# Performance work log

Hardware: AMD Instinct MI355X
Metric: run time of the kernel (lower is better)

## Reference

```python
import jax, jax.numpy as jnp
import numpy as np

NEG_SLOPE = 0.2  # PyG GATConv default leaky_relu slope


def _gat_conv(x, src, dst, W, a_src, a_dst, b, num_nodes, heads, out_dim):
    # x: [N, F_in] -> h: [N, H, C]
    h = (x @ W).reshape(num_nodes, heads, out_dim)
    alpha_src = jnp.sum(h * a_src, axis=-1)  # [N, H]
    alpha_dst = jnp.sum(h * a_dst, axis=-1)  # [N, H]
    # per-edge unnormalized attention logits [E, H]
    alpha = jax.nn.leaky_relu(alpha_src[src] + alpha_dst[dst], NEG_SLOPE)
    # segment softmax over incoming edges of each destination node
    amax = jax.ops.segment_max(alpha, dst, num_segments=num_nodes)  # [N, H]
    e = jnp.exp(alpha - amax[dst])
    denom = jax.ops.segment_sum(e, dst, num_segments=num_nodes)  # [N, H]
    attn = e / denom[dst]  # every node has a self-loop, denom > 0
    # scatter-aggregate messages [E, H, C] -> [N, H, C]
    msg = h[src] * attn[:, :, None]
    out = jax.ops.segment_sum(msg, dst, num_segments=num_nodes)
    return out.reshape(num_nodes, heads * out_dim) + b


def setup_inputs() -> dict:
    key = jax.random.key(0)
    ks = jax.random.split(key, 12)
    N, F_in, H, C1, C2 = 100000, 128, 4, 32, 16
    E = 1600000
    x = jax.random.normal(ks[0], (N, F_in), dtype=jnp.float32)
    edge_index = jax.random.randint(ks[1], (2, E), 0, N, dtype=jnp.int64)
    s1 = 1.0 / np.sqrt(F_in)
    s2 = 1.0 / np.sqrt(H * C1)
    W1 = jax.random.normal(ks[2], (F_in, H * C1), dtype=jnp.float32) * s1
    a_src1 = jax.random.normal(ks[3], (H, C1), dtype=jnp.float32) * s1
    a_dst1 = jax.random.normal(ks[4], (H, C1), dtype=jnp.float32) * s1
    b1 = jnp.zeros((H * C1,), dtype=jnp.float32)
    W2 = jax.random.normal(ks[5], (H * C1, C2), dtype=jnp.float32) * s2
    a_src2 = jax.random.normal(ks[6], (1, C2), dtype=jnp.float32) * s2
    a_dst2 = jax.random.normal(ks[7], (1, C2), dtype=jnp.float32) * s2
    b2 = jnp.zeros((C2,), dtype=jnp.float32)
    return {"x": x, "edge_index": edge_index, "W1": W1, "a_src1": a_src1,
            "a_dst1": a_dst1, "b1": b1, "W2": W2, "a_src2": a_src2,
            "a_dst2": a_dst2, "b2": b2}


def reference(x, edge_index, W1, a_src1, a_dst1, b1, W2, a_src2, a_dst2, b2):
    N = x.shape[0]
    H, C1 = a_src1.shape
    C2 = a_src2.shape[1]
    # PyG GATConv default add_self_loops=True
    loop = jnp.arange(N, dtype=edge_index.dtype)
    src = jnp.concatenate([edge_index[0], loop])
    dst = jnp.concatenate([edge_index[1], loop])
    # dropout_ratio=0.0 / eval mode -> F.dropout is identity
    h = _gat_conv(x, src, dst, W1, a_src1, a_dst1, b1, N, H, C1)
    h = jax.nn.elu(h)
    out = _gat_conv(h, src, dst, W2, a_src2, a_dst2, b2, N, 1, C2)
    return out
```

## Files before the change

### kernel.cpp

```cpp
#include <hip/hip_runtime.h>
#include <cstdint>
#include <cstddef>

#define NEG_SLOPE 0.2f


__device__ __forceinline__ int edge_at(const void* ei, long long idx, int is64) {
    if (is64) return (int)((const long long*)ei)[idx];
    return ((const int*)ei)[idx];
}

__global__ void detect_fmt_kernel(const void* ei, int* flag) {
    if (threadIdx.x == 0 && blockIdx.x == 0) {
        const unsigned* u = (const unsigned*)ei;
        int zc = 0;
        for (int i = 0; i < 128; ++i) zc += (u[2 * i + 1] == 0u);
        *flag = (zc >= 100) ? 1 : 0;
    }
}

__global__ __launch_bounds__(256) void gemm1_kernel(
    const float* __restrict__ x, const float* __restrict__ W,
    const float* __restrict__ a_src, const float* __restrict__ a_dst,
    float* __restrict__ h1, float* __restrict__ asrc, float* __restrict__ adst,
    int N) {
    __shared__ float As2[32][132];
    __shared__ float Bs[32][128];
    const int tid = threadIdx.x;
    const int tx = tid & 15, ty = tid >> 4;
    const int base = blockIdx.x * 128;

    float acc[8][8];
#pragma unroll
    for (int i = 0; i < 8; ++i)
#pragma unroll
        for (int j = 0; j < 8; ++j) acc[i][j] = 0.f;

    for (int kb = 0; kb < 128; kb += 32) {
        {
            const int r0 = tid >> 3;
            const int q  = tid & 7;
#pragma unroll
            for (int p = 0; p < 4; ++p) {
                int r = r0 + p * 32;
                int gr = base + r;
                float4 v = make_float4(0.f, 0.f, 0.f, 0.f);
                if (gr < N) v = *(const float4*)(x + (size_t)gr * 128 + kb + q * 4);
                As2[q * 4 + 0][r] = v.x; As2[q * 4 + 1][r] = v.y;
                As2[q * 4 + 2][r] = v.z; As2[q * 4 + 3][r] = v.w;
            }
        }
        {
            const int k0 = tid >> 5;
            const int f  = tid & 31;
#pragma unroll
            for (int p = 0; p < 4; ++p) {
                int kk = k0 + p * 8;
                float4 v = *(const float4*)(W + (size_t)(kb + kk) * 128 + f * 4);
                *(float4*)&Bs[kk][f * 4] = v;
            }
        }
        __syncthreads();
#pragma unroll 4
        for (int kk = 0; kk < 32; ++kk) {
            float4 a0 = *(const float4*)&As2[kk][ty * 8];
            float4 a1 = *(const float4*)&As2[kk][ty * 8 + 4];
            float a[8] = {a0.x, a0.y, a0.z, a0.w, a1.x, a1.y, a1.z, a1.w};
            float4 b0 = *(const float4*)&Bs[kk][tx * 4];
            float4 b1 = *(const float4*)&Bs[kk][64 + tx * 4];
            float b[8] = {b0.x, b0.y, b0.z, b0.w, b1.x, b1.y, b1.z, b1.w};
#pragma unroll
            for (int i = 0; i < 8; ++i)
#pragma unroll
                for (int j = 0; j < 8; ++j)
                    acc[i][j] = fmaf(a[i], b[j], acc[i][j]);
        }
        __syncthreads();
    }

    float asv[8], adv[8];
#pragma unroll
    for (int jj = 0; jj < 4; ++jj) {
        asv[jj]     = a_src[tx * 4 + jj];
        asv[4 + jj] = a_src[64 + tx * 4 + jj];
        adv[jj]     = a_dst[tx * 4 + jj];
        adv[4 + jj] = a_dst[64 + tx * 4 + jj];
    }

#pragma unroll
    for (int i = 0; i < 8; ++i) {
        int gr = base + ty * 8 + i;
        float p0s = 0.f, p1s = 0.f, p0d = 0.f, p1d = 0.f;
#pragma unroll
        for (int jj = 0; jj < 4; ++jj) {
            p0s = fmaf(acc[i][jj],     asv[jj],     p0s);
            p0d = fmaf(acc[i][jj],     adv[jj],     p0d);
            p1s = fmaf(acc[i][4 + jj], asv[4 + jj], p1s);
            p1d = fmaf(acc[i][4 + jj], adv[4 + jj], p1d);
        }
#pragma unroll
        for (int off = 1; off < 8; off <<= 1) {
            p0s += __shfl_xor(p0s, off);
            p0d += __shfl_xor(p0d, off);
            p1s += __shfl_xor(p1s, off);
            p1d += __shfl_xor(p1d, off);
        }
        if (gr < N) {
            float4 o0 = make_float4(acc[i][0], acc[i][1], acc[i][2], acc[i][3]);
            float4 o1 = make_float4(acc[i][4], acc[i][5], acc[i][6], acc[i][7]);
            *(float4*)(h1 + (size_t)gr * 128 + tx * 4) = o0;
            *(float4*)(h1 + (size_t)gr * 128 + 64 + tx * 4) = o1;
            if ((tx & 7) == 0) {
                int hlo = tx >> 3;
                asrc[gr * 4 + hlo]     = p0s;
                adst[gr * 4 + hlo]     = p0d;
                asrc[gr * 4 + 2 + hlo] = p1s;
                adst[gr * 4 + 2 + hlo] = p1d;
            }
        }
    }
}

__global__ void deg_init_kernel(int* deg, int* cursor, int N) {
    int i = blockIdx.x * 256 + threadIdx.x;
    if (i < N) { deg[i] = 1; cursor[i] = 0; }
}

__global__ void hist_kernel(const void* ei, int* deg, int E, const int* flag) {
    int i = blockIdx.x * 256 + threadIdx.x;
    if (i < E) {
        int is64 = *flag;
        int d = edge_at(ei, (long long)E + i, is64);
        atomicAdd(&deg[d], 1);
    }
}

__global__ void reduce_kernel(const int* __restrict__ deg, int* bsums, int N) {
    __shared__ int s[256];
    int tid = threadIdx.x;
    int base = blockIdx.x * 1024 + tid * 4;
    int t = 0;
#pragma unroll
    for (int u = 0; u < 4; ++u) { int idx = base + u; if (idx < N) t += deg[idx]; }
    s[tid] = t;
    __syncthreads();
    for (int off = 128; off; off >>= 1) {
        if (tid < off) s[tid] += s[tid + off];
        __syncthreads();
    }
    if (tid == 0) bsums[blockIdx.x] = s[0];
}

__global__ void scan_bsums_kernel(int* bsums, int* rowptr, int nb, int N) {
    __shared__ int s[128];
    __shared__ int carry;
    int tid = threadIdx.x;
    if (tid == 0) carry = 0;
    __syncthreads();
    for (int base = 0; base < nb; base += 128) {
        int idx = base + tid;
        int v = (idx < nb) ? bsums[idx] : 0;
        s[tid] = v;
        __syncthreads();
        for (int off = 1; off < 128; off <<= 1) {
            int t = (tid >= off) ? s[tid - off] : 0;
            __syncthreads();
            s[tid] += t;
            __syncthreads();
        }
        int excl = carry + ((tid == 0) ? 0 : s[tid - 1]);
        if (idx < nb) bsums[idx] = excl;
        __syncthreads();
        if (tid == 0) carry += s[127];
        __syncthreads();
    }
    if (tid == 0) rowptr[N] = carry;
}

__global__ void scan_write_kernel(const int* __restrict__ deg,
                                  const int* __restrict__ bsums,
                                  int* __restrict__ rowptr, int N) {
    __shared__ int s[256];
    int tid = threadIdx.x;
    int base_i = blockIdx.x * 1024 + tid * 4;
    int v[4]; int t = 0;
#pragma unroll
    for (int u = 0; u < 4; ++u) {
        int idx = base_i + u;
        v[u] = (idx < N) ? deg[idx] : 0;
        t += v[u];
    }
    s[tid] = t;
    __syncthreads();
    for (int off = 1; off < 256; off <<= 1) {
        int tv = (tid >= off) ? s[tid - off] : 0;
        __syncthreads();
        s[tid] += tv;
        __syncthreads();
    }
    int excl = (tid == 0) ? 0 : s[tid - 1];
    int p = bsums[blockIdx.x] + excl;
#pragma unroll
    for (int u = 0; u < 4; ++u) {
        int idx = base_i + u;
        if (idx < N) rowptr[idx] = p;
        p += v[u];
    }
}

__global__ void scatter_kernel(const void* ei, const int* __restrict__ rowptr,
                               int* cursor, int* __restrict__ srcs,
                               int E, int ET, const int* flag) {
    int i = blockIdx.x * 256 + threadIdx.x;
    if (i < ET) {
        int is64 = *flag;
        int s, d;
        if (i < E) {
            s = edge_at(ei, i, is64);
            d = edge_at(ei, (long long)E + i, is64);
        } else {
            s = d = i - E;
        }
        int pos = rowptr[d] + atomicAdd(&cursor[d], 1);
        srcs[pos] = s;
    }
}

__global__ __launch_bounds__(128) void agg1_kernel(
    const float* __restrict__ h1, const float* __restrict__ asrc,
    const float* __restrict__ adst, const int* __restrict__ rowptr,
    const int* __restrict__ srcs, const float* __restrict__ b1,
    float* __restrict__ g, int N) {
    __shared__ float2 ws[4][36];
    int d = blockIdx.x;
    int tid = threadIdx.x;
    int h = tid >> 5, l = tid & 31;
    int start = rowptr[d], end = rowptr[d + 1];
    int deg = end - start;
    float ad = adst[d * 4 + h];

    float m = -1e30f;
    for (int j = start + l; j < end; j += 32) {
        float t = asrc[srcs[j] * 4 + h] + ad;
        t = (t > 0.f) ? t : NEG_SLOPE * t;
        m = fmaxf(m, t);
    }
#pragma unroll
    for (int off = 16; off; off >>= 1) m = fmaxf(m, __shfl_xor(m, off, 32));

    float a0 = 0.f, a1 = 0.f, a2 = 0.f, a3 = 0.f;
    float a4 = 0.f, a5 = 0.f, a6 = 0.f, a7 = 0.f;
    float lsum = 0.f;
    const float* h1c = h1 + tid;
    for (int cb = 0; cb < deg; cb += 32) {
        int cl = min(32, deg - cb);
        float wv = 0.f; int sv = 0;
        if (l < cl) {
            sv = srcs[start + cb + l];
            float t = asrc[sv * 4 + h] + ad;
            t = (t > 0.f) ? t : NEG_SLOPE * t;
            wv = __expf(t - m);
        }
        ws[h][l] = make_float2(wv, __int_as_float(sv));
        lsum += wv;
        int e = 0;
        for (; e + 8 <= cl; e += 8) {
            float2 p0 = ws[h][e + 0], p1 = ws[h][e + 1];
            float2 p2 = ws[h][e + 2], p3 = ws[h][e + 3];
            float2 p4 = ws[h][e + 4], p5 = ws[h][e + 5];
            float2 p6 = ws[h][e + 6], p7 = ws[h][e + 7];
            a0 = fmaf(p0.x, h1c[(size_t)__float_as_int(p0.y) * 128], a0);
            a1 = fmaf(p1.x, h1c[(size_t)__float_as_int(p1.y) * 128], a1);
            a2 = fmaf(p2.x, h1c[(size_t)__float_as_int(p2.y) * 128], a2);
            a3 = fmaf(p3.x, h1c[(size_t)__float_as_int(p3.y) * 128], a3);
            a4 = fmaf(p4.x, h1c[(size_t)__float_as_int(p4.y) * 128], a4);
            a5 = fmaf(p5.x, h1c[(size_t)__float_as_int(p5.y) * 128], a5);
            a6 = fmaf(p6.x, h1c[(size_t)__float_as_int(p6.y) * 128], a6);
            a7 = fmaf(p7.x, h1c[(size_t)__float_as_int(p7.y) * 128], a7);
        }
        for (; e < cl; ++e) {
            float2 p = ws[h][e];
            a0 = fmaf(p.x, h1c[(size_t)__float_as_int(p.y) * 128], a0);
        }
    }
#pragma unroll
    for (int off = 16; off; off >>= 1) lsum += __shfl_xor(lsum, off, 32);
    float acc = ((a0 + a1) + (a2 + a3)) + ((a4 + a5) + (a6 + a7));
    float r = acc / lsum + b1[tid];
    g[(size_t)d * 128 + tid] = (r > 0.f) ? r : expm1f(r);
}

__global__ __launch_bounds__(256) void gemm2_kernel(
    const float* __restrict__ g, const float* __restrict__ W2,
    const float* __restrict__ a_src2, const float* __restrict__ a_dst2,
    float* __restrict__ h2, float* __restrict__ asrc2, float* __restrict__ adst2,
    int N) {
    __shared__ float W2s[128 * 16];
    __shared__ float gs[16][132];
    int tid = threadIdx.x;
#pragma unroll
    for (int u = 0; u < 8; ++u) W2s[u * 256 + tid] = W2[u * 256 + tid];
    int base = blockIdx.x * 16;
#pragma unroll
    for (int p = 0; p < 2; ++p) {
        int q = tid + p * 256;
        int r = q >> 5, c4 = q & 31;
        int gr = base + r;
        float4 v = make_float4(0.f, 0.f, 0.f, 0.f);
        if (gr < N) v = *(const float4*)(g + (size_t)gr * 128 + c4 * 4);
        *(float4*)&gs[r][c4 * 4] = v;
    }
    __syncthreads();
    int ln = tid >> 4, c = tid & 15;
    int n = base + ln;
    float acc = 0.f;
#pragma unroll 8
    for (int k = 0; k < 128; ++k)
        acc = fmaf(gs[ln][k], W2s[k * 16 + c], acc);
    float s1 = acc * a_src2[c];
    float s2 = acc * a_dst2[c];
#pragma unroll
    for (int off = 8; off; off >>= 1) {
        s1 += __shfl_xor(s1, off, 16);
        s2 += __shfl_xor(s2, off, 16);
    }
    if (n < N) {
        h2[(size_t)n * 16 + c] = acc;
        if (c == 0) { asrc2[n] = s1; adst2[n] = s2; }
    }
}

__global__ __launch_bounds__(256) void agg2_kernel(
    const float* __restrict__ h2, const float* __restrict__ asrc2,
    const float* __restrict__ adst2, const int* __restrict__ rowptr,
    const int* __restrict__ srcs, const float* __restrict__ b2,
    float* __restrict__ out, int N) {
    __shared__ float2 ws2[16][20];
    int tid = threadIdx.x;
    int grp = tid >> 4;
    int d = blockIdx.x * 16 + grp;
    int c = tid & 15;
    if (d >= N) return;
    int start = rowptr[d], end = rowptr[d + 1];
    int deg = end - start;
    float ad = adst2[d];

    float m = -1e30f;
    for (int j = start + c; j < end; j += 16) {
        float t = asrc2[srcs[j]] + ad;
        t = (t > 0.f) ? t : NEG_SLOPE * t;
        m = fmaxf(m, t);
    }
#pragma unroll
    for (int off = 8; off; off >>= 1) m = fmaxf(m, __shfl_xor(m, off, 16));

    float a0 = 0.f, a1 = 0.f, a2 = 0.f, a3 = 0.f;
    float a4 = 0.f, a5 = 0.f, a6 = 0.f, a7 = 0.f;
    float lsum = 0.f;
    const float* h2c = h2 + c;
    for (int cb = 0; cb < deg; cb += 16) {
        int cl = min(16, deg - cb);
        float wv = 0.f; int sv = 0;
        if (c < cl) {
            sv = srcs[start + cb + c];
            float t = asrc2[sv] + ad;
            t = (t > 0.f) ? t : NEG_SLOPE * t;
            wv = __expf(t - m);
        }
        ws2[grp][c] = make_float2(wv, __int_as_float(sv));
        lsum += wv;
        int e = 0;
        for (; e + 8 <= cl; e += 8) {
            float2 p0 = ws2[grp][e + 0], p1 = ws2[grp][e + 1];
            float2 p2 = ws2[grp][e + 2], p3 = ws2[grp][e + 3];
            float2 p4 = ws2[grp][e + 4], p5 = ws2[grp][e + 5];
            float2 p6 = ws2[grp][e + 6], p7 = ws2[grp][e + 7];
            a0 = fmaf(p0.x, h2c[(size_t)__float_as_int(p0.y) * 16], a0);
            a1 = fmaf(p1.x, h2c[(size_t)__float_as_int(p1.y) * 16], a1);
            a2 = fmaf(p2.x, h2c[(size_t)__float_as_int(p2.y) * 16], a2);
            a3 = fmaf(p3.x, h2c[(size_t)__float_as_int(p3.y) * 16], a3);
            a4 = fmaf(p4.x, h2c[(size_t)__float_as_int(p4.y) * 16], a4);
            a5 = fmaf(p5.x, h2c[(size_t)__float_as_int(p5.y) * 16], a5);
            a6 = fmaf(p6.x, h2c[(size_t)__float_as_int(p6.y) * 16], a6);
            a7 = fmaf(p7.x, h2c[(size_t)__float_as_int(p7.y) * 16], a7);
        }
        for (; e < cl; ++e) {
            float2 p = ws2[grp][e];
            a0 = fmaf(p.x, h2c[(size_t)__float_as_int(p.y) * 16], a0);
        }
    }
#pragma unroll
    for (int off = 8; off; off >>= 1) lsum += __shfl_xor(lsum, off, 16);
    float acc = ((a0 + a1) + (a2 + a3)) + ((a4 + a5) + (a6 + a7));
    out[(size_t)d * 16 + c] = acc / lsum + b2[c];
}

extern "C" void kernel_launch(void* const* d_in, const int* in_sizes, int n_in,
                              void* d_out, int out_size, void* d_ws, size_t ws_size,
                              hipStream_t stream) {
    const float* x      = (const float*)d_in[0];
    const void*  ei     = d_in[1];
    const float* W1     = (const float*)d_in[2];
    const float* a_src1 = (const float*)d_in[3];
    const float* a_dst1 = (const float*)d_in[4];
    const float* b1     = (const float*)d_in[5];
    const float* W2     = (const float*)d_in[6];
    const float* a_src2 = (const float*)d_in[7];
    const float* a_dst2 = (const float*)d_in[8];
    const float* b2     = (const float*)d_in[9];

    const int N  = in_sizes[0] / 128;
    const int E  = in_sizes[1] / 2;
    const int ET = E + N;

    char* w = (char*)d_ws;
    size_t off = 0;
    auto alloc = [&](size_t bytes) -> char* {
        char* p = w + off;
        off = (off + bytes + 255) & ~(size_t)255;
        return p;
    };
    float* h1     = (float*)alloc((size_t)N * 128 * 4);
    float* g      = (float*)alloc((size_t)N * 128 * 4);
    float* asrc1  = (float*)alloc((size_t)N * 4 * 4);
    float* adst1  = (float*)alloc((size_t)N * 4 * 4);
    int*   deg    = (int*)alloc((size_t)N * 4);
    int*   cursor = (int*)alloc((size_t)N * 4);
    int*   rowptr = (int*)alloc((size_t)(N + 1) * 4);
    int*   srcs   = (int*)alloc((size_t)ET * 4);
    int*   bsums  = (int*)alloc(4096);
    int*   flag   = (int*)alloc(256);
    float* h2    = h1;
    float* asrc2 = h1 + (size_t)N * 16;
    float* adst2 = asrc2 + N;

    const int nb = (N + 1023) / 1024;

    detect_fmt_kernel<<<1, 1, 0, stream>>>(ei, flag);
    gemm1_kernel<<<(N + 127) / 128, 256, 0, stream>>>(x, W1, a_src1, a_dst1,
                                                      h1, asrc1, adst1, N);
    deg_init_kernel<<<(N + 255) / 256, 256, 0, stream>>>(deg, cursor, N);
    hist_kernel<<<(E + 255) / 256, 256, 0, stream>>>(ei, deg, E, flag);
    reduce_kernel<<<nb, 256, 0, stream>>>(deg, bsums, N);
    scan_bsums_kernel<<<1, 128, 0, stream>>>(bsums, rowptr, nb, N);
    scan_write_kernel<<<nb, 256, 0, stream>>>(deg, bsums, rowptr, N);
    scatter_kernel<<<(ET + 255) / 256, 256, 0, stream>>>(ei, rowptr, cursor, srcs, E, ET, flag);
    agg1_kernel<<<N, 128, 0, stream>>>(h1, asrc1, adst1, rowptr, srcs, b1, g, N);
    gemm2_kernel<<<(N + 15) / 16, 256, 0, stream>>>(g, W2, a_src2, a_dst2, h2, asrc2, adst2, N);
    agg2_kernel<<<(N + 15) / 16, 256, 0, stream>>>(h2, asrc2, adst2, rowptr, srcs, b2, (float*)d_out, N);
}
```

Measured before the change: 542.3 us.

## Process one node per wavefront in agg1 with float2 gathers

Restructures the layer-1 aggregation so each 64-lane wavefront handles one destination node, with 16 lanes per head and each lane owning two channels loaded as float2. Four nodes share a 256-thread block instead of one node per 128-thread block. The aim is to cut per-block overhead, halve the number of gather instructions, and improve occupancy. In exchange, edge chunks shrink to 16, so there are more chunk iterations and shuffles for high-degree nodes.

```diff
diff --git a/kernel.cpp b/kernel.cpp
--- a/kernel.cpp
+++ b/kernel.cpp
@@ -226,68 +226,87 @@
     }
 }
 
-__global__ __launch_bounds__(128) void agg1_kernel(
+__global__ __launch_bounds__(256, 8) void agg1_kernel(
     const float* __restrict__ h1, const float* __restrict__ asrc,
     const float* __restrict__ adst, const int* __restrict__ rowptr,
     const int* __restrict__ srcs, const float* __restrict__ b1,
     float* __restrict__ g, int N) {
-    __shared__ float2 ws[4][36];
-    int d = blockIdx.x;
-    int tid = threadIdx.x;
-    int h = tid >> 5, l = tid & 31;
+    __shared__ float2 ws[4][4][18];
+    int tid = threadIdx.x;
+    int wid = tid >> 6;
+    int w   = tid & 63;
+    int d   = blockIdx.x * 4 + wid;
+    if (d >= N) return;
+    int h   = w >> 4;
+    int el  = w & 15;
+    int c0  = 2 * w;
     int start = rowptr[d], end = rowptr[d + 1];
     int deg = end - start;
     float ad = adst[d * 4 + h];
 
     float m = -1e30f;
-    for (int j = start + l; j < end; j += 32) {
+    for (int j = start + el; j < end; j += 16) {
         float t = asrc[srcs[j] * 4 + h] + ad;
         t = (t > 0.f) ? t : NEG_SLOPE * t;
         m = fmaxf(m, t);
     }
 #pragma unroll
-    for (int off = 16; off; off >>= 1) m = fmaxf(m, __shfl_xor(m, off, 32));
-
-    float a0 = 0.f, a1 = 0.f, a2 = 0.f, a3 = 0.f;
-    float a4 = 0.f, a5 = 0.f, a6 = 0.f, a7 = 0.f;
+    for (int off = 8; off; off >>= 1) m = fmaxf(m, __shfl_xor(m, off, 16));
+
+    float2 a0 = {0.f, 0.f}, a1 = {0.f, 0.f}, a2 = {0.f, 0.f}, a3 = {0.f, 0.f};
+    float2 a4 = {0.f, 0.f}, a5 = {0.f, 0.f}, a6 = {0.f, 0.f}, a7 = {0.f, 0.f};
     float lsum = 0.f;
-    const float* h1c = h1 + tid;
-    for (int cb = 0; cb < deg; cb += 32) {
-        int cl = min(32, deg - cb);
+    const float* h1c = h1 + c0;
+    for (int cb = 0; cb < deg; cb += 16) {
+        int cl = min(16, deg - cb);
         float wv = 0.f; int sv = 0;
-        if (l < cl) {
-            sv = srcs[start + cb + l];
+        if (el < cl) {
+            sv = srcs[start + cb + el];
             float t = asrc[sv * 4 + h] + ad;
             t = (t > 0.f) ? t : NEG_SLOPE * t;
             wv = __expf(t - m);
         }
-        ws[h][l] = make_float2(wv, __int_as_float(sv));
+        ws[wid][h][el] = make_float2(wv, __int_as_float(sv));
         lsum += wv;
         int e = 0;
         for (; e + 8 <= cl; e += 8) {
-            float2 p0 = ws[h][e + 0], p1 = ws[h][e + 1];
-            float2 p2 = ws[h][e + 2], p3 = ws[h][e + 3];
-            float2 p4 = ws[h][e + 4], p5 = ws[h][e + 5];
-            float2 p6 = ws[h][e + 6], p7 = ws[h][e + 7];
-            a0 = fmaf(p0.x, h1c[(size_t)__float_as_int(p0.y) * 128], a0);
-            a1 = fmaf(p1.x, h1c[(size_t)__float_as_int(p1.y) * 128], a1);
-            a2 = fmaf(p2.x, h1c[(size_t)__float_as_int(p2.y) * 128], a2);
-            a3 = fmaf(p3.x, h1c[(size_t)__float_as_int(p3.y) * 128], a3);
-            a4 = fmaf(p4.x, h1c[(size_t)__float_as_int(p4.y) * 128], a4);
-            a5 = fmaf(p5.x, h1c[(size_t)__float_as_int(p5.y) * 128], a5);
-            a6 = fmaf(p6.x, h1c[(size_t)__float_as_int(p6.y) * 128], a6);
-            a7 = fmaf(p7.x, h1c[(size_t)__float_as_int(p7.y) * 128], a7);
+            float2 p0 = ws[wid][h][e + 0], p1 = ws[wid][h][e + 1];
+            float2 p2 = ws[wid][h][e + 2], p3 = ws[wid][h][e + 3];
+            float2 p4 = ws[wid][h][e + 4], p5 = ws[wid][h][e + 5];
+            float2 p6 = ws[wid][h][e + 6], p7 = ws[wid][h][e + 7];
+            float2 v0 = *(const float2*)(h1c + (size_t)__float_as_int(p0.y) * 128);
+            float2 v1 = *(const float2*)(h1c + (size_t)__float_as_int(p1.y) * 128);
+            float2 v2 = *(const float2*)(h1c + (size_t)__float_as_int(p2.y) * 128);
+            float2 v3 = *(const float2*)(h1c + (size_t)__float_as_int(p3.y) * 128);
+            float2 v4 = *(const float2*)(h1c + (size_t)__float_as_int(p4.y) * 128);
+            float2 v5 = *(const float2*)(h1c + (size_t)__float_as_int(p5.y) * 128);
+            float2 v6 = *(const float2*)(h1c + (size_t)__float_as_int(p6.y) * 128);
+            float2 v7 = *(const float2*)(h1c + (size_t)__float_as_int(p7.y) * 128);
+            a0.x = fmaf(p0.x, v0.x, a0.x); a0.y = fmaf(p0.x, v0.y, a0.y);
+            a1.x = fmaf(p1.x, v1.x, a1.x); a1.y = fmaf(p1.x, v1.y, a1.y);
+            a2.x = fmaf(p2.x, v2.x, a2.x); a2.y = fmaf(p2.x, v2.y, a2.y);
+            a3.x = fmaf(p3.x, v3.x, a3.x); a3.y = fmaf(p3.x, v3.y, a3.y);
+            a4.x = fmaf(p4.x, v4.x, a4.x); a4.y = fmaf(p4.x, v4.y, a4.y);
+            a5.x = fmaf(p5.x, v5.x, a5.x); a5.y = fmaf(p5.x, v5.y, a5.y);
+            a6.x = fmaf(p6.x, v6.x, a6.x); a6.y = fmaf(p6.x, v6.y, a6.y);
+            a7.x = fmaf(p7.x, v7.x, a7.x); a7.y = fmaf(p7.x, v7.y, a7.y);
         }
         for (; e < cl; ++e) {
-            float2 p = ws[h][e];
-            a0 = fmaf(p.x, h1c[(size_t)__float_as_int(p.y) * 128], a0);
-        }
-    }
-#pragma unroll
-    for (int off = 16; off; off >>= 1) lsum += __shfl_xor(lsum, off, 32);
-    float acc = ((a0 + a1) + (a2 + a3)) + ((a4 + a5) + (a6 + a7));
-    float r = acc / lsum + b1[tid];
-    g[(size_t)d * 128 + tid] = (r > 0.f) ? r : expm1f(r);
+            float2 p = ws[wid][h][e];
+            float2 v = *(const float2*)(h1c + (size_t)__float_as_int(p.y) * 128);
+            a0.x = fmaf(p.x, v.x, a0.x); a0.y = fmaf(p.x, v.y, a0.y);
+        }
+    }
+#pragma unroll
+    for (int off = 8; off; off >>= 1) lsum += __shfl_xor(lsum, off, 16);
+    float accx = ((a0.x + a1.x) + (a2.x + a3.x)) + ((a4.x + a5.x) + (a6.x + a7.x));
+    float accy = ((a0.y + a1.y) + (a2.y + a3.y)) + ((a4.y + a5.y) + (a6.y + a7.y));
+    float2 bb = *(const float2*)(b1 + c0);
+    float r0 = accx / lsum + bb.x;
+    float r1 = accy / lsum + bb.y;
+    r0 = (r0 > 0.f) ? r0 : expm1f(r0);
+    r1 = (r1 > 0.f) ? r1 : expm1f(r1);
+    *(float2*)(g + (size_t)d * 128 + c0) = make_float2(r0, r1);
 }
 
 __global__ __launch_bounds__(256) void gemm2_kernel(
@@ -445,7 +464,7 @@
     scan_bsums_kernel<<<1, 128, 0, stream>>>(bsums, rowptr, nb, N);
     scan_write_kernel<<<nb, 256, 0, stream>>>(deg, bsums, rowptr, N);
     scatter_kernel<<<(ET + 255) / 256, 256, 0, stream>>>(ei, rowptr, cursor, srcs, E, ET, flag);
-    agg1_kernel<<<N, 128, 0, stream>>>(h1, asrc1, adst1, rowptr, srcs, b1, g, N);
+    agg1_kernel<<<(N + 3) / 4, 256, 0, stream>>>(h1, asrc1, adst1, rowptr, srcs, b1, g, N);
     gemm2_kernel<<<(N + 15) / 16, 256, 0, stream>>>(g, W2, a_src2, a_dst2, h2, asrc2, adst2, N);
     agg2_kernel<<<(N + 15) / 16, 256, 0, stream>>>(h2, asrc2, adst2, rowptr, srcs, b2, (float*)d_out, N);
 }
```

Measured after the change: 541.6 us. No clear change (-0.1%).

## Fuse layer-2 linear projection into layer-1 aggregation epilogue

Applied to the files above, without the earlier changes.

Removes the separate gemm2 kernel. Each agg1 block now multiplies its ELU output row by W2 in shared memory and writes h2 plus the layer-2 attention scalars directly, avoiding the write and re-read of the N×128 intermediate g. h2 is moved to a separate buffer, since h1 is still being read by other blocks. Edge weights and source indices are now broadcast with wave shuffles instead of staged through shared memory. In exchange, each block re-reads W2 from global/cache, adds extra block syncs, and does a small per-node matvec with low parallel efficiency.

```diff
diff --git a/kernel.cpp b/kernel.cpp
--- a/kernel.cpp
+++ b/kernel.cpp
@@ -230,8 +230,11 @@
     const float* __restrict__ h1, const float* __restrict__ asrc,
     const float* __restrict__ adst, const int* __restrict__ rowptr,
     const int* __restrict__ srcs, const float* __restrict__ b1,
-    float* __restrict__ g, int N) {
-    __shared__ float2 ws[4][36];
+    const float* __restrict__ W2, const float* __restrict__ a_src2,
+    const float* __restrict__ a_dst2, float* __restrict__ h2,
+    float* __restrict__ asrc2, float* __restrict__ adst2, int N) {
+    __shared__ float gs[128];
+    __shared__ float red[32];
     int d = blockIdx.x;
     int tid = threadIdx.x;
     int h = tid >> 5, l = tid & 31;
@@ -261,72 +264,60 @@
             t = (t > 0.f) ? t : NEG_SLOPE * t;
             wv = __expf(t - m);
         }
-        ws[h][l] = make_float2(wv, __int_as_float(sv));
         lsum += wv;
         int e = 0;
         for (; e + 8 <= cl; e += 8) {
-            float2 p0 = ws[h][e + 0], p1 = ws[h][e + 1];
-            float2 p2 = ws[h][e + 2], p3 = ws[h][e + 3];
-            float2 p4 = ws[h][e + 4], p5 = ws[h][e + 5];
-            float2 p6 = ws[h][e + 6], p7 = ws[h][e + 7];
-            a0 = fmaf(p0.x, h1c[(size_t)__float_as_int(p0.y) * 128], a0);
-            a1 = fmaf(p1.x, h1c[(size_t)__float_as_int(p1.y) * 128], a1);
-            a2 = fmaf(p2.x, h1c[(size_t)__float_as_int(p2.y) * 128], a2);
-            a3 = fmaf(p3.x, h1c[(size_t)__float_as_int(p3.y) * 128], a3);
-            a4 = fmaf(p4.x, h1c[(size_t)__float_as_int(p4.y) * 128], a4);
-            a5 = fmaf(p5.x, h1c[(size_t)__float_as_int(p5.y) * 128], a5);
-            a6 = fmaf(p6.x, h1c[(size_t)__float_as_int(p6.y) * 128], a6);
-            a7 = fmaf(p7.x, h1c[(size_t)__float_as_int(p7.y) * 128], a7);
+            int  s0 = __shfl(sv, e + 0, 32), s1 = __shfl(sv, e + 1, 32);
+            int  s2 = __shfl(sv, e + 2, 32), s3 = __shfl(sv, e + 3, 32);
+            int  s4 = __shfl(sv, e + 4, 32), s5 = __shfl(sv, e + 5, 32);
+            int  s6 = __shfl(sv, e + 6, 32), s7 = __shfl(sv, e + 7, 32);
+            float w0 = __shfl(wv, e + 0, 32), w1 = __shfl(wv, e + 1, 32);
+            float w2 = __shfl(wv, e + 2, 32), w3 = __shfl(wv, e + 3, 32);
+            float w4 = __shfl(wv, e + 4, 32), w5 = __shfl(wv, e + 5, 32);
+            float w6 = __shfl(wv, e + 6, 32), w7 = __shfl(wv, e + 7, 32);
+            a0 = fmaf(w0, h1c[(size_t)s0 * 128], a0);
+            a1 = fmaf(w1, h1c[(size_t)s1 * 128], a1);
+            a2 = fmaf(w2, h1c[(size_t)s2 * 128], a2);
+            a3 = fmaf(w3, h1c[(size_t)s3 * 128], a3);
+            a4 = fmaf(w4, h1c[(size_t)s4 * 128], a4);
+            a5 = fmaf(w5, h1c[(size_t)s5 * 128], a5);
+            a6 = fmaf(w6, h1c[(size_t)s6 * 128], a6);
+            a7 = fmaf(w7, h1c[(size_t)s7 * 128], a7);
         }
         for (; e < cl; ++e) {
-            float2 p = ws[h][e];
-            a0 = fmaf(p.x, h1c[(size_t)__float_as_int(p.y) * 128], a0);
+            int s = __shfl(sv, e, 32);
+            float w = __shfl(wv, e, 32);
+            a0 = fmaf(w, h1c[(size_t)s * 128], a0);
         }
     }
 #pragma unroll
     for (int off = 16; off; off >>= 1) lsum += __shfl_xor(lsum, off, 32);
     float acc = ((a0 + a1) + (a2 + a3)) + ((a4 + a5) + (a6 + a7));
     float r = acc / lsum + b1[tid];
-    g[(size_t)d * 128 + tid] = (r > 0.f) ? r : expm1f(r);
-}
-
-__global__ __launch_bounds__(256) void gemm2_kernel(
-    const float* __restrict__ g, const float* __restrict__ W2,
-    const float* __restrict__ a_src2, const float* __restrict__ a_dst2,
-    float* __restrict__ h2, float* __restrict__ asrc2, float* __restrict__ adst2,
-    int N) {
-    __shared__ float W2s[128 * 16];
-    __shared__ float gs[16][132];
-    int tid = threadIdx.x;
-#pragma unroll
-    for (int u = 0; u < 8; ++u) W2s[u * 256 + tid] = W2[u * 256 + tid];
-    int base = blockIdx.x * 16;
-#pragma unroll
-    for (int p = 0; p < 2; ++p) {
-        int q = tid + p * 256;
-        int r = q >> 5, c4 = q & 31;
-        int gr = base + r;
-        float4 v = make_float4(0.f, 0.f, 0.f, 0.f);
-        if (gr < N) v = *(const float4*)(g + (size_t)gr * 128 + c4 * 4);
-        *(float4*)&gs[r][c4 * 4] = v;
-    }
+    r = (r > 0.f) ? r : expm1f(r);
+
+    gs[tid] = r;
     __syncthreads();
-    int ln = tid >> 4, c = tid & 15;
-    int n = base + ln;
-    float acc = 0.f;
-#pragma unroll 8
-    for (int k = 0; k < 128; ++k)
-        acc = fmaf(gs[ln][k], W2s[k * 16 + c], acc);
-    float s1 = acc * a_src2[c];
-    float s2 = acc * a_dst2[c];
-#pragma unroll
-    for (int off = 8; off; off >>= 1) {
-        s1 += __shfl_xor(s1, off, 16);
-        s2 += __shfl_xor(s2, off, 16);
-    }
-    if (n < N) {
-        h2[(size_t)n * 16 + c] = acc;
-        if (c == 0) { asrc2[n] = s1; adst2[n] = s2; }
+    int c = tid & 15, sl = tid >> 4;
+    float p = 0.f;
+#pragma unroll
+    for (int kk = 0; kk < 16; ++kk)
+        p = fmaf(gs[sl * 16 + kk], W2[(sl * 16 + kk) * 16 + c], p);
+    p += __shfl_xor(p, 16);
+    p += __shfl_xor(p, 32);
+    if ((tid & 63) < 16) red[(tid >> 6) * 16 + c] = p;
+    __syncthreads();
+    if (tid < 16) {
+        float hv = red[tid] + red[16 + tid];
+        h2[(size_t)d * 16 + tid] = hv;
+        float s1 = hv * a_src2[tid];
+        float s2 = hv * a_dst2[tid];
+#pragma unroll
+        for (int off = 8; off; off >>= 1) {
+            s1 += __shfl_xor(s1, off, 16);
+            s2 += __shfl_xor(s2, off, 16);
+        }
+        if (tid == 0) { asrc2[d] = s1; adst2[d] = s2; }
     }
 }
 
@@ -421,7 +412,7 @@
         return p;
     };
     float* h1     = (float*)alloc((size_t)N * 128 * 4);
-    float* g      = (float*)alloc((size_t)N * 128 * 4);
+    float* l2buf  = (float*)alloc((size_t)N * 128 * 4);
     float* asrc1  = (float*)alloc((size_t)N * 4 * 4);
     float* adst1  = (float*)alloc((size_t)N * 4 * 4);
     int*   deg    = (int*)alloc((size_t)N * 4);
@@ -430,8 +421,8 @@
     int*   srcs   = (int*)alloc((size_t)ET * 4);
     int*   bsums  = (int*)alloc(4096);
     int*   flag   = (int*)alloc(256);
-    float* h2    = h1;
-    float* asrc2 = h1 + (size_t)N * 16;
+    float* h2    = l2buf;
+    float* asrc2 = l2buf + (size_t)N * 16;
     float* adst2 = asrc2 + N;
 
     const int nb = (N + 1023) / 1024;
@@ -445,7 +436,7 @@
     scan_bsums_kernel<<<1, 128, 0, stream>>>(bsums, rowptr, nb, N);
     scan_write_kernel<<<nb, 256, 0, stream>>>(deg, bsums, rowptr, N);
     scatter_kernel<<<(ET + 255) / 256, 256, 0, stream>>>(ei, rowptr, cursor, srcs, E, ET, flag);
-    agg1_kernel<<<N, 128, 0, stream>>>(h1, asrc1, adst1, rowptr, srcs, b1, g, N);
-    gemm2_kernel<<<(N + 15) / 16, 256, 0, stream>>>(g, W2, a_src2, a_dst2, h2, asrc2, adst2, N);
+    agg1_kernel<<<N, 128, 0, stream>>>(h1, asrc1, adst1, rowptr, srcs, b1,
+                                       W2, a_src2, a_dst2, h2, asrc2, adst2, N);
     agg2_kernel<<<(N + 15) / 16, 256, 0, stream>>>(h2, asrc2, adst2, rowptr, srcs, b2, (float*)d_out, N);
 }
```

After: 523.4 us. 3.5% less time.
